# Optimization experiments

Measured on AMD Instinct MI355X. Metric: run time of the kernel, lower is better.

## Reference

```python
import jax, jax.numpy as jnp
import numpy as np

BATCH = 8
N_POINTS = 2048
HOP = 1  # hop_length


def setup_inputs() -> dict:
    key = jax.random.key(0)
    kx = jax.random.fold_in(key, 0)
    x = jax.random.normal(kx, (BATCH, N_POINTS), dtype=jnp.float32)
    # learnable window-width parameter (init_lambd = 20.0)
    lambd = jnp.full((1,), 20.0, dtype=jnp.float32)
    return {"x": x, "lambd": lambd}


def reference(x, lambd):
    """Batched differentiable Gaussian-window spectrogram.

    Equivalent to looping over the batch and calling
    tf.differentiable_spectrogram(x[i] - mean(x[i]), |lambd|, hop_length=HOP):
    a Gaussian window over the WHOLE signal centered at t_c = 0, HOP, ..., n,
    followed by a zero-padded one-sided FFT (n_fft = 2n) and power spectrum.
    Output: (B, 1, n+1, n//HOP + 1).
    """
    B, n = x.shape
    sigma = jnp.abs(lambd)[0]
    # per-sample mean subtraction
    x = x - jnp.mean(x, axis=1, keepdims=True)
    t = jnp.arange(n, dtype=jnp.float32)                       # (n,)
    t_c = jnp.arange(0, n + 1, HOP, dtype=jnp.float32)         # (F,) frame centers
    # Gaussian windows over the whole signal, one per frame center: (F, n)
    windows = jnp.exp(-0.5 * jnp.square((t[None, :] - t_c[:, None]) / sigma))
    # windowed signals: (B, F, n)
    xw = x[:, None, :] * windows[None, :, :]
    # zero-padded one-sided FFT -> n+1 frequency bins: (B, F, n+1)
    spec = jnp.fft.rfft(xw, n=2 * n, axis=-1)
    power = spec.real ** 2 + spec.imag ** 2                    # power spectrogram
    # (B, 1, n+1 freq, F time)
    return jnp.swapaxes(power, 1, 2)[:, None, :, :]
```

## Files before the change

kernel.cpp:

```cpp
#include <hip/hip_runtime.h>
#include <math.h>

#define NPTS    2048
#define NBINS   2049
#define NFRAMES 2049
#define U       320
#define PAD     160
#define XPLEN   2560

#define MTOT    4224
#define MBLK    33
#define NBLK    17
#define BM      128
#define BN      128
#define SPAN    448
#define SSTRIDE 464
#define ASTRIDE 72

typedef __attribute__((ext_vector_type(8))) short short8_t;
typedef __attribute__((ext_vector_type(4))) short short4_t;
typedef __attribute__((ext_vector_type(4))) float float4_t;

static __device__ __forceinline__ unsigned short f2bf(float f) {
    unsigned u = __float_as_uint(f);
    unsigned r = (u + 0x7fffu + ((u >> 16) & 1u)) >> 16;
    return (unsigned short)r;
}

__global__ void mean_kernel(const float* __restrict__ x, float* __restrict__ means) {
    __shared__ float red[256];
    const int b = blockIdx.x;
    float s = 0.f;
    for (int t = threadIdx.x; t < NPTS; t += 256) s += x[b * NPTS + t];
    red[threadIdx.x] = s;
    __syncthreads();
    for (int off = 128; off > 0; off >>= 1) {
        if (threadIdx.x < off) red[threadIdx.x] += red[threadIdx.x + off];
        __syncthreads();
    }
    if (threadIdx.x == 0) means[b] = red[0] * (1.f / (float)NPTS);
}

__global__ void xpgen_kernel(const float* __restrict__ x, const float* __restrict__ means,
                             unsigned short* __restrict__ xp) {
    const int idx = blockIdx.x * 256 + threadIdx.x;
    const int b = idx / XPLEN;
    const int t = idx - b * XPLEN;
    float v = 0.f;
    const int s = t - PAD;
    if (s >= 0 && s < NPTS) v = x[b * NPTS + s] - means[b];
    xp[idx] = f2bf(v);
}

__global__ void wgen_kernel(const float* __restrict__ lambd, unsigned short* __restrict__ W) {
    const int idx = blockIdx.x * 256 + threadIdx.x;
    if (idx >= MTOT * U) return;
    const int m = idx / U;
    const int u = idx - m * U;
    const int k = m >> 1, p = m & 1;
    float val = 0.f;
    if (k < NBINS) {
        const float sigma = fabsf(lambd[0]);
        const float uc = (float)(u - PAD);
        const float g = __expf(-0.5f * uc * uc / (sigma * sigma));
        const float ph = (float)M_PI * (float)k * uc * (1.f / 2048.f);
        float sn, cs;
        sincosf(ph, &sn, &cs);
        val = g * (p ? sn : cs);
    }
    W[idx] = f2bf(val);
}

__global__ __launch_bounds__(256) void spec_mfma(
        const unsigned short* __restrict__ W, const unsigned short* __restrict__ xp,
        float* __restrict__ out) {
    __shared__ unsigned short Alds[BM * ASTRIDE];
    __shared__ unsigned short span[4 * SSTRIDE];

    const int tid = threadIdx.x;
    const int b  = blockIdx.z;
    const int n0 = blockIdx.x * BN;
    const int m0 = blockIdx.y * BM;

    {
        const unsigned short* xpb = xp + b * XPLEN;
        for (int i = tid; i < 4 * SPAN; i += 256) {
            const int c = i / SPAN;
            const int t = i - c * SPAN;
            span[c * SSTRIDE + t] = xpb[n0 + t + c];
        }
    }

    const int lane = tid & 63;
    const int wv   = tid >> 6;
    const int wm   = (wv & 1) * 64;
    const int wn   = (wv >> 1) * 64;
    const int col  = lane & 15;
    const int q    = lane >> 4;

    float4_t acc[4][4];
    #pragma unroll
    for (int mt = 0; mt < 4; ++mt)
        #pragma unroll
        for (int nt = 0; nt < 4; ++nt)
            acc[mt][nt] = (float4_t){0.f, 0.f, 0.f, 0.f};

    const unsigned short* bptr[4];
    #pragma unroll
    for (int nt = 0; nt < 4; ++nt) {
        const int n = wn + nt * 16 + col;
        const int c = n & 3;
        bptr[nt] = span + c * SSTRIDE + (8 * q + n - c);
    }

    const int row  = tid >> 1;
    const int half = tid & 1;
    const unsigned short* wrow = W + (size_t)(m0 + row) * U + half * 32;
    float4* l4 = (float4*)(Alds + row * ASTRIDE + half * 32);

    #pragma unroll
    for (int s = 0; s < 5; ++s) {
        const int kb = s * 64;
        const float4* g4 = (const float4*)(wrow + kb);
        float4 r0 = g4[0], r1 = g4[1], r2 = g4[2], r3 = g4[3];
        __syncthreads();
        l4[0] = r0; l4[1] = r1; l4[2] = r2; l4[3] = r3;
        __syncthreads();

        #pragma unroll
        for (int ks = 0; ks < 2; ++ks) {
            const int kk = ks * 32;
            short8_t af[4], bf[4];
            #pragma unroll
            for (int mt = 0; mt < 4; ++mt)
                af[mt] = *(const short8_t*)(Alds + (wm + mt * 16 + col) * ASTRIDE + kk + q * 8);
            #pragma unroll
            for (int nt = 0; nt < 4; ++nt) {
                const unsigned short* p = bptr[nt] + kb + kk;
                short4_t lo = *(const short4_t*)(p);
                short4_t hi = *(const short4_t*)(p + 4);
                bf[nt] = __builtin_shufflevector(lo, hi, 0, 1, 2, 3, 4, 5, 6, 7);
            }
            #pragma unroll
            for (int mt = 0; mt < 4; ++mt)
                #pragma unroll
                for (int nt = 0; nt < 4; ++nt)
                    acc[mt][nt] = __builtin_amdgcn_mfma_f32_16x16x32_bf16(
                        af[mt], bf[nt], acc[mt][nt], 0, 0, 0);
        }
    }

    const int fbase = n0 + wn + col;
    #pragma unroll
    for (int mt = 0; mt < 4; ++mt) {
        const int mrow = m0 + wm + mt * 16 + q * 4;
        const int kk0  = mrow >> 1;
        #pragma unroll
        for (int nt = 0; nt < 4; ++nt) {
            const int f = fbase + nt * 16;
            if (f < NFRAMES) {
                const float4_t a = acc[mt][nt];
                const float p0 = a[0] * a[0] + a[1] * a[1];
                const float p1 = a[2] * a[2] + a[3] * a[3];
                if (kk0 < NBINS)
                    out[((size_t)b * NBINS + kk0) * NFRAMES + f] = p0;
                if (kk0 + 1 < NBINS)
                    out[((size_t)b * NBINS + kk0 + 1) * NFRAMES + f] = p1;
            }
        }
    }
}

extern "C" void kernel_launch(void* const* d_in, const int* in_sizes, int n_in,
                              void* d_out, int out_size, void* d_ws, size_t ws_size,
                              hipStream_t stream) {
    const float* x     = (const float*)d_in[0];
    const float* lambd = (const float*)d_in[1];
    float*       out   = (float*)d_out;

    char* ws = (char*)d_ws;
    float*          means = (float*)ws;
    unsigned short* xp    = (unsigned short*)(ws + 256);
    unsigned short* W     = (unsigned short*)(ws + 41216);

    hipLaunchKernelGGL(mean_kernel, dim3(8), dim3(256), 0, stream, x, means);
    hipLaunchKernelGGL(xpgen_kernel, dim3(8 * XPLEN / 256), dim3(256), 0, stream,
                       x, means, xp);
    hipLaunchKernelGGL(wgen_kernel, dim3((MTOT * U + 255) / 256), dim3(256), 0, stream,
                       lambd, W);

    dim3 grid(NBLK, MBLK, 8);
    hipLaunchKernelGGL(spec_mfma, grid, dim3(256), 0, stream, W, xp, out);
}
```

Before: 190.9 us.

## Widen GEMM N-tile, double-buffer A tiles, fuse prep kernels, use recurrence window gen

The spectrogram GEMM now uses 256-wide frame tiles with eight accumulators per wave, double-buffers the W tile in LDS and prefetches the next global chunk into registers. The mean and padded-signal kernels are merged into one launch. Window generation computes 64 consecutive entries per thread using sincos and Gaussian recurrences instead of one sincosf and exp per element. The aim is to cut launch count, barriers and transcendental work, at the cost of higher register pressure, a grid of fewer blocks, and accumulated rounding in the recurrences.

```diff
diff --git a/kernel.cpp b/kernel.cpp
--- a/kernel.cpp
+++ b/kernel.cpp
@@ -6,16 +6,18 @@
 #define NFRAMES 2049
 #define U       320
 #define PAD     160
-#define XPLEN   2560
+#define XPLEN   2688
 
 #define MTOT    4224
 #define MBLK    33
-#define NBLK    17
+#define NBLK    9
 #define BM      128
-#define BN      128
-#define SPAN    448
-#define SSTRIDE 464
+#define BN      256
+#define BK      64
+#define SPAN    (BN + U)
+#define SSTRIDE 592
 #define ASTRIDE 72
+#define ABUF    (BM * ASTRIDE)
 
 typedef __attribute__((ext_vector_type(8))) short short8_t;
 typedef __attribute__((ext_vector_type(4))) short short4_t;
@@ -27,7 +29,7 @@
     return (unsigned short)r;
 }
 
-__global__ void mean_kernel(const float* __restrict__ x, float* __restrict__ means) {
+__global__ void prep_kernel(const float* __restrict__ x, unsigned short* __restrict__ xp) {
     __shared__ float red[256];
     const int b = blockIdx.x;
     float s = 0.f;
@@ -38,43 +40,53 @@
         if (threadIdx.x < off) red[threadIdx.x] += red[threadIdx.x + off];
         __syncthreads();
     }
-    if (threadIdx.x == 0) means[b] = red[0] * (1.f / (float)NPTS);
-}
-
-__global__ void xpgen_kernel(const float* __restrict__ x, const float* __restrict__ means,
-                             unsigned short* __restrict__ xp) {
-    const int idx = blockIdx.x * 256 + threadIdx.x;
-    const int b = idx / XPLEN;
-    const int t = idx - b * XPLEN;
-    float v = 0.f;
-    const int s = t - PAD;
-    if (s >= 0 && s < NPTS) v = x[b * NPTS + s] - means[b];
-    xp[idx] = f2bf(v);
-}
-
+    const float mean = red[0] * (1.f / (float)NPTS);
+    for (int t = threadIdx.x; t < XPLEN; t += 256) {
+        const int s2 = t - PAD;
+        float v = (s2 >= 0 && s2 < NPTS) ? (x[b * NPTS + s2] - mean) : 0.f;
+        xp[b * XPLEN + t] = f2bf(v);
+    }
+}
+
+#define WCH 5
 __global__ void wgen_kernel(const float* __restrict__ lambd, unsigned short* __restrict__ W) {
     const int idx = blockIdx.x * 256 + threadIdx.x;
-    if (idx >= MTOT * U) return;
-    const int m = idx / U;
-    const int u = idx - m * U;
+    if (idx >= MTOT * WCH) return;
+    const int m  = idx / WCH;
+    const int ch = idx - m * WCH;
     const int k = m >> 1, p = m & 1;
-    float val = 0.f;
-    if (k < NBINS) {
-        const float sigma = fabsf(lambd[0]);
-        const float uc = (float)(u - PAD);
-        const float g = __expf(-0.5f * uc * uc / (sigma * sigma));
-        const float ph = (float)M_PI * (float)k * uc * (1.f / 2048.f);
-        float sn, cs;
-        sincosf(ph, &sn, &cs);
-        val = g * (p ? sn : cs);
-    }
-    W[idx] = f2bf(val);
-}
-
-__global__ __launch_bounds__(256) void spec_mfma(
+    unsigned int* wp = (unsigned int*)(W + (size_t)m * U + ch * 64);
+    if (k >= NBINS) {
+        #pragma unroll
+        for (int j = 0; j < 32; ++j) wp[j] = 0u;
+        return;
+    }
+    const float sigma  = fabsf(lambd[0]);
+    const float inv2s2 = 0.5f / (sigma * sigma);
+    const float u0 = (float)(ch * 64 - PAD);
+    const float dphi = (float)M_PI * (float)k * (1.f / 2048.f);
+    float sn, cs, sd, cd;
+    sincosf(dphi * u0, &sn, &cs);
+    sincosf(dphi, &sd, &cd);
+    float       g  = __expf(-u0 * u0 * inv2s2);
+    float       gr = __expf(-(2.f * u0 + 1.f) * inv2s2);
+    const float gq = __expf(-2.f * inv2s2);
+    #pragma unroll
+    for (int j = 0; j < 32; ++j) {
+        unsigned short lo = f2bf(g * (p ? sn : cs));
+        float cn = cs * cd - sn * sd; sn = fmaf(sn, cd, cs * sd); cs = cn;
+        g *= gr; gr *= gq;
+        unsigned short hi = f2bf(g * (p ? sn : cs));
+        cn = cs * cd - sn * sd; sn = fmaf(sn, cd, cs * sd); cs = cn;
+        g *= gr; gr *= gq;
+        wp[j] = (unsigned int)lo | ((unsigned int)hi << 16);
+    }
+}
+
+__global__ __launch_bounds__(256, 2) void spec_mfma(
         const unsigned short* __restrict__ W, const unsigned short* __restrict__ xp,
         float* __restrict__ out) {
-    __shared__ unsigned short Alds[BM * ASTRIDE];
+    __shared__ unsigned short Alds[2 * ABUF];
     __shared__ unsigned short span[4 * SSTRIDE];
 
     const int tid = threadIdx.x;
@@ -94,49 +106,58 @@
     const int lane = tid & 63;
     const int wv   = tid >> 6;
     const int wm   = (wv & 1) * 64;
-    const int wn   = (wv >> 1) * 64;
+    const int wn   = (wv >> 1) * 128;
     const int col  = lane & 15;
     const int q    = lane >> 4;
-
-    float4_t acc[4][4];
-    #pragma unroll
-    for (int mt = 0; mt < 4; ++mt)
-        #pragma unroll
-        for (int nt = 0; nt < 4; ++nt)
-            acc[mt][nt] = (float4_t){0.f, 0.f, 0.f, 0.f};
-
-    const unsigned short* bptr[4];
-    #pragma unroll
-    for (int nt = 0; nt < 4; ++nt) {
-        const int n = wn + nt * 16 + col;
-        const int c = n & 3;
-        bptr[nt] = span + c * SSTRIDE + (8 * q + n - c);
-    }
 
     const int row  = tid >> 1;
     const int half = tid & 1;
     const unsigned short* wrow = W + (size_t)(m0 + row) * U + half * 32;
-    float4* l4 = (float4*)(Alds + row * ASTRIDE + half * 32);
+    const int lbase = row * ASTRIDE + half * 32;
+
+    const int cc = col & 3;
+    const unsigned short* bbase = span + cc * SSTRIDE + (wn + col - cc) + 8 * q;
+
+    float4_t acc[4][8];
+    #pragma unroll
+    for (int mt = 0; mt < 4; ++mt)
+        #pragma unroll
+        for (int nt = 0; nt < 8; ++nt)
+            acc[mt][nt] = (float4_t){0.f, 0.f, 0.f, 0.f};
+
+    float4 r0, r1, r2, r3;
+    {
+        const float4* g4 = (const float4*)(wrow);
+        r0 = g4[0]; r1 = g4[1]; r2 = g4[2]; r3 = g4[3];
+        float4* l4 = (float4*)(Alds + lbase);
+        l4[0] = r0; l4[1] = r1; l4[2] = r2; l4[3] = r3;
+        const float4* g5 = (const float4*)(wrow + BK);
+        r0 = g5[0]; r1 = g5[1]; r2 = g5[2]; r3 = g5[3];
+    }
+    __syncthreads();
 
     #pragma unroll
     for (int s = 0; s < 5; ++s) {
-        const int kb = s * 64;
-        const float4* g4 = (const float4*)(wrow + kb);
-        float4 r0 = g4[0], r1 = g4[1], r2 = g4[2], r3 = g4[3];
-        __syncthreads();
-        l4[0] = r0; l4[1] = r1; l4[2] = r2; l4[3] = r3;
-        __syncthreads();
-
+        if (s < 4) {
+            float4* l4 = (float4*)(Alds + ((s + 1) & 1) * ABUF + lbase);
+            l4[0] = r0; l4[1] = r1; l4[2] = r2; l4[3] = r3;
+        }
+        if (s < 3) {
+            const float4* g4 = (const float4*)(wrow + (s + 2) * BK);
+            r0 = g4[0]; r1 = g4[1]; r2 = g4[2]; r3 = g4[3];
+        }
+        const unsigned short* cur = Alds + (s & 1) * ABUF;
+        const int kb = s * BK;
         #pragma unroll
         for (int ks = 0; ks < 2; ++ks) {
             const int kk = ks * 32;
-            short8_t af[4], bf[4];
+            short8_t af[4], bf[8];
             #pragma unroll
             for (int mt = 0; mt < 4; ++mt)
-                af[mt] = *(const short8_t*)(Alds + (wm + mt * 16 + col) * ASTRIDE + kk + q * 8);
+                af[mt] = *(const short8_t*)(cur + (wm + mt * 16 + col) * ASTRIDE + kk + q * 8);
             #pragma unroll
-            for (int nt = 0; nt < 4; ++nt) {
-                const unsigned short* p = bptr[nt] + kb + kk;
+            for (int nt = 0; nt < 8; ++nt) {
+                const unsigned short* p = bbase + nt * 16 + kb + kk;
                 short4_t lo = *(const short4_t*)(p);
                 short4_t hi = *(const short4_t*)(p + 4);
                 bf[nt] = __builtin_shufflevector(lo, hi, 0, 1, 2, 3, 4, 5, 6, 7);
@@ -144,10 +165,11 @@
             #pragma unroll
             for (int mt = 0; mt < 4; ++mt)
                 #pragma unroll
-                for (int nt = 0; nt < 4; ++nt)
+                for (int nt = 0; nt < 8; ++nt)
                     acc[mt][nt] = __builtin_amdgcn_mfma_f32_16x16x32_bf16(
                         af[mt], bf[nt], acc[mt][nt], 0, 0, 0);
         }
+        __syncthreads();
     }
 
     const int fbase = n0 + wn + col;
@@ -156,7 +178,7 @@
         const int mrow = m0 + wm + mt * 16 + q * 4;
         const int kk0  = mrow >> 1;
         #pragma unroll
-        for (int nt = 0; nt < 4; ++nt) {
+        for (int nt = 0; nt < 8; ++nt) {
             const int f = fbase + nt * 16;
             if (f < NFRAMES) {
                 const float4_t a = acc[mt][nt];
@@ -179,14 +201,11 @@
     float*       out   = (float*)d_out;
 
     char* ws = (char*)d_ws;
-    float*          means = (float*)ws;
-    unsigned short* xp    = (unsigned short*)(ws + 256);
-    unsigned short* W     = (unsigned short*)(ws + 41216);
-
-    hipLaunchKernelGGL(mean_kernel, dim3(8), dim3(256), 0, stream, x, means);
-    hipLaunchKernelGGL(xpgen_kernel, dim3(8 * XPLEN / 256), dim3(256), 0, stream,
-                       x, means, xp);
-    hipLaunchKernelGGL(wgen_kernel, dim3((MTOT * U + 255) / 256), dim3(256), 0, stream,
+    unsigned short* xp = (unsigned short*)ws;
+    unsigned short* W  = (unsigned short*)(ws + 43264);
+
+    hipLaunchKernelGGL(prep_kernel, dim3(8), dim3(256), 0, stream, x, xp);
+    hipLaunchKernelGGL(wgen_kernel, dim3((MTOT * WCH + 255) / 256), dim3(256), 0, stream,
                        lambd, W);
 
     dim3 grid(NBLK, MBLK, 8);
```

New measurement: 187.6 us. No clear change (-1.7%).
